# Optimization experiments

Measured on AMD Instinct MI355X. Metric: run time of the kernel, lower is better.

## Reference

```python
import jax, jax.numpy as jnp
import numpy as np

L, H, E, T, B, V = 8, 16, 1024, 1024, 2, 800
D = E // H  # head_size = 64
STD = 0.02


def setup_inputs() -> dict:
    key = jax.random.key(0)
    ks = iter(jax.random.split(key, 32))

    def nrm(shape):
        return jax.random.normal(next(ks), shape, jnp.float32) * STD

    latlong = jax.random.uniform(next(ks), (B, T, 2), jnp.float32)
    wl = jax.random.uniform(next(ks), (B, T, 1), jnp.float32, minval=3.0, maxval=11.0)
    inp = {
        "idx": jnp.concatenate([latlong, wl], axis=-1),  # [B,T,3]
        "tok_table": nrm((V, E)),
        "pos_W": nrm((2, E)),
        "pos_b": jnp.zeros((E,), jnp.float32),
        # stacked per-layer params (per-head q/k/v linears fused into [E,E])
        "Wq": nrm((L, E, E)),
        "Wk": nrm((L, E, E)),
        "Wv": nrm((L, E, E)),
        "Wo": nrm((L, E, E)),
        "bo": jnp.zeros((L, E), jnp.float32),
        "W1": nrm((L, E, 4 * E)),
        "b1": jnp.zeros((L, 4 * E), jnp.float32),
        "W2": nrm((L, 4 * E, E)),
        "b2": jnp.zeros((L, E), jnp.float32),
        "ln1_g": jnp.ones((L, E), jnp.float32),
        "ln1_b": jnp.zeros((L, E), jnp.float32),
        "ln2_g": jnp.ones((L, E), jnp.float32),
        "ln2_b": jnp.zeros((L, E), jnp.float32),
        "lnf_g": jnp.ones((E,), jnp.float32),
        "lnf_b": jnp.zeros((E,), jnp.float32),
        "lm_W": nrm((E, V)),
        "lm_b": jnp.zeros((V,), jnp.float32),
    }
    return inp


def _ln(x, g, b, eps=1e-5):
    m = x.mean(-1, keepdims=True)
    v = x.var(-1, keepdims=True)
    return (x - m) * jax.lax.rsqrt(v + eps) * g + b


def _block(x, p):
    Wq, Wk, Wv, Wo, bo, W1, b1, W2, b2, g1, be1, g2, be2 = p
    Bx, Tx, _ = x.shape
    h = _ln(x, g1, be1)
    q = (h @ Wq).reshape(Bx, Tx, H, D)
    k = (h @ Wk).reshape(Bx, Tx, H, D)
    v = (h @ Wv).reshape(Bx, Tx, H, D)
    scores = jnp.einsum('bqhd,bkhd->bhqk', q, k) * (D ** -0.5)
    mask = jnp.tril(jnp.ones((Tx, Tx), bool))  # causal
    scores = jnp.where(mask, scores, -jnp.inf)
    w = jax.nn.softmax(scores, axis=-1)  # dropout=0 (eval) -> identity
    attn = jnp.einsum('bhqk,bkhd->bqhd', w, v).reshape(Bx, Tx, E)
    x = x + attn @ Wo + bo
    h = _ln(x, g2, be2)
    x = x + jax.nn.relu(h @ W1 + b1) @ W2 + b2
    return x


def reference(idx, tok_table, pos_W, pos_b, Wq, Wk, Wv, Wo, bo, W1, b1, W2, b2,
              ln1_g, ln1_b, ln2_g, ln2_b, lnf_g, lnf_b, lm_W, lm_b):
    # water level channel -> token id in [0, V-1]
    idx_wl = jnp.clip(jnp.round(idx[..., 2] * 100.0 - 300.0), 0, V - 1).astype(jnp.int32)
    tok_emb = tok_table[idx_wl]                      # [B,T,E]
    pos_emb = idx[..., :2] @ pos_W + pos_b           # [B,T,E]
    x = tok_emb + pos_emb

    params = (Wq, Wk, Wv, Wo, bo, W1, b1, W2, b2, ln1_g, ln1_b, ln2_g, ln2_b)

    def body(carry, p):
        return _block(carry, p), None

    x, _ = jax.lax.scan(body, x, params)
    x = _ln(x, lnf_g, lnf_b)
    logits = x @ lm_W + lm_b                         # [B,T,V]
    return logits
```

## Files before the change

kernel.cpp:

```cpp
#include <hip/hip_runtime.h>
#include <hip/hip_bf16.h>

#define L_ 8
#define H_ 16
#define E_ 1024
#define T_ 1024
#define B_ 2
#define V_ 800
#define D_ 64
#define FF_ 4096
#define N_ (B_ * T_)
#define QS_ 3072

typedef unsigned short u16;
typedef __bf16 bf16x8 __attribute__((ext_vector_type(8)));
typedef float f32x4 __attribute__((ext_vector_type(4)));

__device__ __forceinline__ u16 f2b(float f) {
    unsigned int u = __float_as_uint(f);
    unsigned int r = (u + 0x7fffu + ((u >> 16) & 1u)) >> 16;
    return (u16)r;
}

__device__ __forceinline__ void gld16(const u16* g, u16* l) {
    __builtin_amdgcn_global_load_lds(
        (__attribute__((address_space(1))) void*)(uintptr_t)g,
        (__attribute__((address_space(3))) void*)(unsigned)(uintptr_t)l,
        16, 0, 0);
}

__global__ __launch_bounds__(256) void embed_k(
    const float* __restrict__ idx, const float* __restrict__ tok,
    const float* __restrict__ posW, const float* __restrict__ posb,
    float* __restrict__ x)
{
    int row = blockIdx.x;
    int e = threadIdx.x * 4;
    float lat = idx[row * 3 + 0];
    float lon = idx[row * 3 + 1];
    float wl  = idx[row * 3 + 2];
    float tf = rintf(wl * 100.0f - 300.0f);
    tf = fminf(fmaxf(tf, 0.0f), (float)(V_ - 1));
    int tkn = (int)tf;

    float4 tv = *(const float4*)(tok + (size_t)tkn * E_ + e);
    float4 p0 = *(const float4*)(posW + e);
    float4 p1 = *(const float4*)(posW + E_ + e);
    float4 pb = *(const float4*)(posb + e);
    float4 ov;
    ov.x = tv.x + lat * p0.x + lon * p1.x + pb.x;
    ov.y = tv.y + lat * p0.y + lon * p1.y + pb.y;
    ov.z = tv.z + lat * p0.z + lon * p1.z + pb.z;
    ov.w = tv.w + lat * p0.w + lon * p1.w + pb.w;
    *(float4*)(x + (size_t)row * E_ + e) = ov;
}

__global__ __launch_bounds__(256) void ln_k(
    const float* __restrict__ x, const float* __restrict__ g,
    const float* __restrict__ bta, u16* __restrict__ out)
{
    __shared__ float rs[4], rq[4];
    int row = blockIdx.x;
    int tid = threadIdx.x;
    const float* xr = x + (size_t)row * E_;
    float4 xv = *(const float4*)(xr + tid * 4);
    float s = xv.x + xv.y + xv.z + xv.w;
    float q = xv.x * xv.x + xv.y * xv.y + xv.z * xv.z + xv.w * xv.w;
    #pragma unroll
    for (int off = 32; off; off >>= 1) {
        s += __shfl_xor(s, off, 64);
        q += __shfl_xor(q, off, 64);
    }
    int wv = tid >> 6, ln = tid & 63;
    if (ln == 0) { rs[wv] = s; rq[wv] = q; }
    __syncthreads();
    s = rs[0] + rs[1] + rs[2] + rs[3];
    q = rq[0] + rq[1] + rq[2] + rq[3];
    float mean = s * (1.0f / E_);
    float var  = q * (1.0f / E_) - mean * mean;
    float inv  = 1.0f / sqrtf(var + 1e-5f);
    int c = tid * 4;
    float4 gv = *(const float4*)(g + c);
    float4 bv = *(const float4*)(bta + c);
    ushort4 ov;
    ov.x = f2b((xv.x - mean) * inv * gv.x + bv.x);
    ov.y = f2b((xv.y - mean) * inv * gv.y + bv.y);
    ov.z = f2b((xv.z - mean) * inv * gv.z + bv.z);
    ov.w = f2b((xv.w - mean) * inv * gv.w + bv.w);
    *(ushort4*)(out + (size_t)row * E_ + c) = ov;
}

__global__ __launch_bounds__(256) void comb_ln_k(
    const float* __restrict__ Cp, const float* __restrict__ bias,
    float* __restrict__ x, const float* __restrict__ g,
    const float* __restrict__ bta, u16* __restrict__ hout)
{
    __shared__ float rs[4], rq[4];
    int row = blockIdx.x;
    int tid = threadIdx.x;
    int c = tid * 4;
    size_t off = (size_t)row * E_ + c;
    const size_t total = (size_t)N_ * E_;
    float4 p0 = *(const float4*)(Cp + off);
    float4 p1 = *(const float4*)(Cp + total + off);
    float4 p2 = *(const float4*)(Cp + 2 * total + off);
    float4 p3 = *(const float4*)(Cp + 3 * total + off);
    float4 xv = *(const float4*)(x + off);
    float4 bv = *(const float4*)(bias + c);
    xv.x += p0.x + p1.x + p2.x + p3.x + bv.x;
    xv.y += p0.y + p1.y + p2.y + p3.y + bv.y;
    xv.z += p0.z + p1.z + p2.z + p3.z + bv.z;
    xv.w += p0.w + p1.w + p2.w + p3.w + bv.w;
    *(float4*)(x + off) = xv;

    float s = xv.x + xv.y + xv.z + xv.w;
    float q = xv.x * xv.x + xv.y * xv.y + xv.z * xv.z + xv.w * xv.w;
    #pragma unroll
    for (int o = 32; o; o >>= 1) {
        s += __shfl_xor(s, o, 64);
        q += __shfl_xor(q, o, 64);
    }
    int wv = tid >> 6, ln = tid & 63;
    if (ln == 0) { rs[wv] = s; rq[wv] = q; }
    __syncthreads();
    s = rs[0] + rs[1] + rs[2] + rs[3];
    q = rq[0] + rq[1] + rq[2] + rq[3];
    float mean = s * (1.0f / E_);
    float var  = q * (1.0f / E_) - mean * mean;
    float inv  = 1.0f / sqrtf(var + 1e-5f);
    float4 gv = *(const float4*)(g + c);
    float4 bb = *(const float4*)(bta + c);
    ushort4 ov;
    ov.x = f2b((xv.x - mean) * inv * gv.x + bb.x);
    ov.y = f2b((xv.y - mean) * inv * gv.y + bb.y);
    ov.z = f2b((xv.z - mean) * inv * gv.z + bb.z);
    ov.w = f2b((xv.w - mean) * inv * gv.w + bb.w);
    *(ushort4*)(hout + off) = ov;
}

__device__ __forceinline__ void wtrans_body(
    const float* __restrict__ W, u16* __restrict__ Wt, int K, int M,
    int m0, int k0)
{
    __shared__ float tile[64][65];
    int tid = threadIdx.x;
    int rr = tid >> 4, c4 = (tid & 15) * 4;
    if (m0 + 64 <= M) {
        #pragma unroll
        for (int p = 0; p < 4; p++) {
            int kk = rr + p * 16;
            float4 v4 = *(const float4*)(W + (size_t)(k0 + kk) * M + m0 + c4);
            tile[kk][c4 + 0] = v4.x; tile[kk][c4 + 1] = v4.y;
            tile[kk][c4 + 2] = v4.z; tile[kk][c4 + 3] = v4.w;
        }
    } else {
        #pragma unroll
        for (int p = 0; p < 4; p++) {
            int kk = rr + p * 16;
            const float* wr = W + (size_t)(k0 + kk) * M;
            #pragma unroll
            for (int c = 0; c < 4; c++) {
                int m = m0 + c4 + c;
                tile[kk][c4 + c] = (m < M) ? wr[m] : 0.0f;
            }
        }
    }
    __syncthreads();
    #pragma unroll
    for (int p = 0; p < 4; p++) {
        int ml = rr + p * 16;
        ushort4 o;
        o.x = f2b(tile[c4 + 0][ml]);
        o.y = f2b(tile[c4 + 1][ml]);
        o.z = f2b(tile[c4 + 2][ml]);
        o.w = f2b(tile[c4 + 3][ml]);
        *(ushort4*)(Wt + (size_t)(m0 + ml) * K + k0 + c4) = o;
    }
}

__global__ __launch_bounds__(256) void wtrans_k(
    const float* __restrict__ W, u16* __restrict__ Wt, int K, int M)
{
    wtrans_body(W, Wt, K, M, blockIdx.x * 64, blockIdx.y * 64);
}

__global__ __launch_bounds__(256) void wtrans_all_k(
    const float* __restrict__ Wq, const float* __restrict__ Wk,
    const float* __restrict__ Wv, const float* __restrict__ Wo,
    const float* __restrict__ W1, const float* __restrict__ W2,
    u16* __restrict__ wqkv_t, u16* __restrict__ wo_t,
    u16* __restrict__ w1_t, u16* __restrict__ w2_t)
{
    int bx = blockIdx.x, by = blockIdx.y, z = blockIdx.z;
    const size_t M1 = 1024 * 1024;
    if (z < 4) {
        if (bx >= 16) return;
        const float* W = (z == 0) ? Wq : (z == 1) ? Wk : (z == 2) ? Wv : Wo;
        u16* dst = (z < 3) ? (wqkv_t + (size_t)z * M1) : wo_t;
        wtrans_body(W, dst, E_, E_, bx * 64, by * 64);
    } else if (z == 4) {
        wtrans_body(W1, w1_t, E_, FF_, bx * 64, by * 64);
    } else {
        int id = by * 64 + bx;
        int mb = id >> 6, kb = id & 63;
        wtrans_body(W2, w2_t, FF_, E_, mb * 64, kb * 64);
    }
}

__global__ __launch_bounds__(256) void gemm_bf16(
    const u16* __restrict__ A, const u16* __restrict__ Bt,
    const float* __restrict__ bias, const float* __restrict__ res,
    float* __restrict__ Cf, u16* __restrict__ Cb, float* __restrict__ Cp,
    u16* __restrict__ VtOut, int K, int M, int relu)
{
    __shared__ __align__(16) u16 As[3][128 * 32];
    __shared__ __align__(16) u16 Bs[3][128 * 32];
    int tid = threadIdx.x;
    int bm = blockIdx.y * 128, bn = blockIdx.x * 128;
    int zz = blockIdx.z;
    int kslice = K / (int)gridDim.z;
    int lane = tid & 63, wv = tid >> 6;
    int l15 = lane & 15, q4 = lane >> 4;
    int wm = (wv & 1) * 64, wn = (wv >> 1) * 64;

    const u16* ga = A + (size_t)(bm + (tid >> 2)) * K + zz * kslice + (tid & 3) * 8;
    const u16* gb = Bt + (size_t)(bn + (tid >> 2)) * K + zz * kslice + (tid & 3) * 8;
    size_t gstep = (size_t)64 * K;
    int lofs = wv * (16 * 32);

    f32x4 acc[4][4];
    #pragma unroll
    for (int i = 0; i < 4; i++)
        #pragma unroll
        for (int j = 0; j < 4; j++)
            acc[i][j] = (f32x4){0.0f, 0.0f, 0.0f, 0.0f};

    auto STAGE = [&](int buf, int t) {
        const u16* a0 = ga + t * 32;
        const u16* b0 = gb + t * 32;
        u16* la = &As[buf][0] + lofs;
        u16* lb = &Bs[buf][0] + lofs;
        gld16(a0, la);
        gld16(a0 + gstep, la + 64 * 32);
        gld16(b0, lb);
        gld16(b0 + gstep, lb + 64 * 32);
    };

    int nt = kslice / 32;
    STAGE(0, 0);
    if (nt > 1) STAGE(1, 1);

    for (int t = 0; t < nt; ++t) {
        if (t + 1 < nt)
            asm volatile("s_waitcnt vmcnt(4) lgkmcnt(0)\n\ts_barrier" ::: "memory");
        else
            asm volatile("s_waitcnt vmcnt(0) lgkmcnt(0)\n\ts_barrier" ::: "memory");
        if (t + 2 < nt) STAGE((t + 2) % 3, t + 2);

        int cur = t % 3;
        const bf16x8* Ap = (const bf16x8*)(&As[cur][0]) + (wm + l15) * 4 + q4;
        const bf16x8* Bp = (const bf16x8*)(&Bs[cur][0]) + (wn + l15) * 4 + q4;
        bf16x8 af[4], bg[4];
        #pragma unroll
        for (int i = 0; i < 4; i++) { af[i] = Ap[i * 64]; bg[i] = Bp[i * 64]; }
        #pragma unroll
        for (int i = 0; i < 4; i++)
            #pragma unroll
            for (int j = 0; j < 4; j++)
                acc[i][j] = __builtin_amdgcn_mfma_f32_16x16x32_bf16(
                    af[i], bg[j], acc[i][j], 0, 0, 0);
    }

    size_t poff = (size_t)zz * N_ * M;
    #pragma unroll
    for (int i = 0; i < 4; i++) {
        int r0 = bm + wm + i * 16 + q4 * 4;
        #pragma unroll
        for (int j = 0; j < 4; j++) {
            int col = bn + wn + j * 16 + l15;
            if (col < M) {
                if (Cp) {
                    #pragma unroll
                    for (int r = 0; r < 4; r++)
                        Cp[poff + (size_t)(r0 + r) * M + col] = acc[i][j][r];
                } else {
                    float bv = bias ? bias[col] : 0.0f;
                    u16 vb[4];
                    #pragma unroll
                    for (int r = 0; r < 4; r++) {
                        size_t off = (size_t)(r0 + r) * M + col;
                        float v = acc[i][j][r] + bv;
                        if (res) v += res[off];
                        if (relu) v = fmaxf(v, 0.0f);
                        u16 hv = f2b(v);
                        vb[r] = hv;
                        if (Cb) Cb[off] = hv; else Cf[off] = v;
                    }
                    if (VtOut && col >= 2 * E_) {
                        int vcol = col - 2 * E_;
                        int hh = vcol >> 6, dd = vcol & 63;
                        int bb = r0 >> 10, t0 = r0 & 1023;
                        *(ushort4*)(VtOut +
                            ((size_t)(bb * H_ + hh) * D_ + dd) * T_ + t0) =
                            *(ushort4*)vb;
                    }
                }
            }
        }
    }
}

__global__ __launch_bounds__(256) void combine_k(
    const float* __restrict__ Cp, const float* __restrict__ bias,
    float* __restrict__ Cf, int M, int total)
{
    int e = (blockIdx.x * 256 + threadIdx.x) * 4;
    if (e >= total) return;
    float4 a = *(const float4*)(Cp + e);
    float4 b = *(const float4*)(Cp + (size_t)total + e);
    a.x += b.x; a.y += b.y; a.z += b.z; a.w += b.w;
    int col = e % M;
    if (bias) {
        float4 bv = *(const float4*)(bias + col);
        a.x += bv.x; a.y += bv.y; a.z += bv.z; a.w += bv.w;
    }
    *(float4*)(Cf + e) = a;
}

__global__ __launch_bounds__(256) void attn_mfma_k(
    const u16* __restrict__ QKV, const u16* __restrict__ Vt,
    u16* __restrict__ O)
{
    __shared__ __align__(16) u16 Ps[4][16 * 72];
    int tid = threadIdx.x;
    int wv = tid >> 6, lane = tid & 63;
    int c = lane & 15, q4 = lane >> 4;
    int qb = (int)(gridDim.x - 1) - (int)blockIdx.x;
    int h = blockIdx.y, b = blockIdx.z;
    int q0 = qb * 64 + wv * 16;
    const float scale = 0.125f;

    const u16* qrow = QKV + (size_t)(b * T_ + q0 + c) * QS_ + h * D_;
    bf16x8 qf0 = *(const bf16x8*)(qrow + q4 * 8);
    bf16x8 qf1 = *(const bf16x8*)(qrow + 32 + q4 * 8);

    const u16* kbase  = QKV + (size_t)b * T_ * QS_ + E_ + h * D_;
    const u16* vtbase = Vt + (size_t)(b * H_ + h) * D_ * T_;

    float l_acc[4] = {0.0f, 0.0f, 0.0f, 0.0f};
    f32x4 acc_o[4];
    #pragma unroll
    for (int nt = 0; nt < 4; nt++) acc_o[nt] = (f32x4){0.f, 0.f, 0.f, 0.f};

    u16* ps = &Ps[wv][0];

    for (int kt = 0; kt <= qb; kt++) {
        int k0 = kt * 64;
        bool diag = (kt == qb);

        bf16x8 kf[4][2];
        #pragma unroll
        for (int j = 0; j < 4; j++) {
            const u16* kr = kbase + (size_t)(k0 + 16 * j + c) * QS_ + q4 * 8;
            kf[j][0] = *(const bf16x8*)(kr);
            kf[j][1] = *(const bf16x8*)(kr + 32);
        }

        #pragma unroll
        for (int j = 0; j < 4; j++) {
            f32x4 sa = (f32x4){0.f, 0.f, 0.f, 0.f};
            sa = __builtin_amdgcn_mfma_f32_16x16x32_bf16(qf0, kf[j][0], sa, 0, 0, 0);
            sa = __builtin_amdgcn_mfma_f32_16x16x32_bf16(qf1, kf[j][1], sa, 0, 0, 0);
            #pragma unroll
            for (int r = 0; r < 4; r++) {
                bool masked = diag && (k0 + 16 * j + c > q0 + 4 * q4 + r);
                float pj = masked ? 0.0f : __expf(sa[r] * scale);
                l_acc[r] += pj;
                ps[(4 * q4 + r) * 72 + 16 * j + c] = f2b(pj);
            }
        }
        bf16x8 pf0 = *(const bf16x8*)(ps + c * 72 + q4 * 8);
        bf16x8 pf1 = *(const bf16x8*)(ps + c * 72 + 32 + q4 * 8);

        bf16x8 vf[4][2];
        #pragma unroll
        for (int nt = 0; nt < 4; nt++) {
            const u16* vr = vtbase + (size_t)(16 * nt + c) * T_ + k0 + q4 * 8;
            vf[nt][0] = *(const bf16x8*)(vr);
            vf[nt][1] = *(const bf16x8*)(vr + 32);
        }

        #pragma unroll
        for (int nt = 0; nt < 4; nt++) {
            acc_o[nt] = __builtin_amdgcn_mfma_f32_16x16x32_bf16(pf0, vf[nt][0], acc_o[nt], 0, 0, 0);
            acc_o[nt] = __builtin_amdgcn_mfma_f32_16x16x32_bf16(pf1, vf[nt][1], acc_o[nt], 0, 0, 0);
        }
    }

    #pragma unroll
    for (int r = 0; r < 4; r++) {
        float ts = l_acc[r];
        ts += __shfl_xor(ts, 1, 64);
        ts += __shfl_xor(ts, 2, 64);
        ts += __shfl_xor(ts, 4, 64);
        ts += __shfl_xor(ts, 8, 64);
        l_acc[r] = ts;
    }

    #pragma unroll
    for (int r = 0; r < 4; r++) {
        float inv = 1.0f / l_acc[r];
        size_t orow = (size_t)(b * T_ + q0 + 4 * q4 + r) * E_ + h * D_;
        #pragma unroll
        for (int nt = 0; nt < 4; nt++)
            O[orow + 16 * nt + c] = f2b(acc_o[nt][r] * inv);
    }
}

extern "C" void kernel_launch(void* const* d_in, const int* in_sizes, int n_in,
                              void* d_out, int out_size, void* d_ws, size_t ws_size,
                              hipStream_t stream)
{
    const float* idx   = (const float*)d_in[0];
    const float* tok   = (const float*)d_in[1];
    const float* posW  = (const float*)d_in[2];
    const float* posb  = (const float*)d_in[3];
    const float* Wq    = (const float*)d_in[4];
    const float* Wk    = (const float*)d_in[5];
    const float* Wv    = (const float*)d_in[6];
    const float* Wo    = (const float*)d_in[7];
    const float* bo    = (const float*)d_in[8];
    const float* W1    = (const float*)d_in[9];
    const float* b1    = (const float*)d_in[10];
    const float* W2    = (const float*)d_in[11];
    const float* b2    = (const float*)d_in[12];
    const float* ln1g  = (const float*)d_in[13];
    const float* ln1b  = (const float*)d_in[14];
    const float* ln2g  = (const float*)d_in[15];
    const float* ln2b  = (const float*)d_in[16];
    const float* lnfg  = (const float*)d_in[17];
    const float* lnfb  = (const float*)d_in[18];
    const float* lmW   = (const float*)d_in[19];
    const float* lmb   = (const float*)d_in[20];
    float* out = (float*)d_out;

    const size_t M1 = 1024 * 1024;
    float* ws    = (float*)d_ws;
    float* x     = ws;
    float* cpart = x + 2 * M1;
    u16* qkv   = (u16*)(cpart + 8 * M1);
    u16* vt    = qkv + 6 * M1;
    u16* h_bf  = vt + 2 * M1;
    u16* ao_bf = h_bf + 2 * M1;
    u16* ff_bf = ao_bf + 2 * M1;
    u16* wq_t  = ff_bf + 8 * M1;
    u16* wo_t  = wq_t + 3 * M1;
    u16* w1_t  = wo_t + 1 * M1;
    u16* w2_t  = w1_t + 4 * M1;
    u16* wlm_t = w2_t + 4 * M1;

    dim3 blk(256);
    dim3 gQKV(3072 / 128, N_ / 128, 1);
    dim3 gWo(1024 / 128, N_ / 128, 4);
    dim3 gW1(4096 / 128, N_ / 128, 1);
    dim3 gW2(1024 / 128, N_ / 128, 4);
    dim3 gLM(7, N_ / 128, 2);
    dim3 gAT(T_ / 64, H_, B_);
    dim3 gWT(64, 16, 6);
    dim3 tLM(14, 16);
    int totLM = N_ * V_;
    dim3 cLM(totLM / 4 / 256);

    embed_k<<<N_, blk, 0, stream>>>(idx, tok, posW, posb, x);
    ln_k<<<N_, blk, 0, stream>>>(x, ln1g, ln1b, h_bf);

    for (int l = 0; l < L_; l++) {
        size_t oEE = (size_t)l * E_ * E_;
        size_t oE  = (size_t)l * E_;
        size_t oEF = (size_t)l * E_ * FF_;
        size_t oF  = (size_t)l * FF_;

        wtrans_all_k<<<gWT, blk, 0, stream>>>(
            Wq + oEE, Wk + oEE, Wv + oEE, Wo + oEE, W1 + oEF, W2 + oEF,
            wq_t, wo_t, w1_t, w2_t);
        gemm_bf16<<<gQKV, blk, 0, stream>>>(h_bf, wq_t, nullptr, nullptr,
                                            nullptr, qkv, nullptr, vt, E_, QS_, 0);
        attn_mfma_k<<<gAT, blk, 0, stream>>>(qkv, vt, ao_bf);
        gemm_bf16<<<gWo, blk, 0, stream>>>(ao_bf, wo_t, nullptr, nullptr,
                                           nullptr, nullptr, cpart, nullptr, E_, E_, 0);
        comb_ln_k<<<N_, blk, 0, stream>>>(cpart, bo + oE, x,
                                          ln2g + oE, ln2b + oE, h_bf);
        gemm_bf16<<<gW1, blk, 0, stream>>>(h_bf, w1_t, b1 + oF, nullptr,
                                           nullptr, ff_bf, nullptr, nullptr, E_, FF_, 1);
        gemm_bf16<<<gW2, blk, 0, stream>>>(ff_bf, w2_t, nullptr, nullptr,
                                           nullptr, nullptr, cpart, nullptr, FF_, E_, 0);
        if (l < L_ - 1) {
            comb_ln_k<<<N_, blk, 0, stream>>>(cpart, b2 + oE, x,
                                              ln1g + oE + E_, ln1b + oE + E_, h_bf);
        } else {
            comb_ln_k<<<N_, blk, 0, stream>>>(cpart, b2 + oE, x,
                                              lnfg, lnfb, h_bf);
        }
    }

    wtrans_k<<<tLM, blk, 0, stream>>>(lmW, wlm_t, E_, V_);
    gemm_bf16<<<gLM, blk, 0, stream>>>(h_bf, wlm_t, nullptr, nullptr,
                                       nullptr, nullptr, cpart, nullptr, E_, V_, 0);
    combine_k<<<cLM, blk, 0, stream>>>(cpart, lmb, out, V_, totLM);
}
```

Before: 1.858 ms.

## Batch weight transposes, atomic split-K residual adds, XCD block remap, MFMA priority

```diff
diff --git a/kernel.cpp b/kernel.cpp
--- a/kernel.cpp
+++ b/kernel.cpp
@@ -29,13 +29,16 @@
         16, 0, 0);
 }
 
-__global__ __launch_bounds__(256) void embed_k(
+__global__ __launch_bounds__(256) void embed_ln_k(
     const float* __restrict__ idx, const float* __restrict__ tok,
     const float* __restrict__ posW, const float* __restrict__ posb,
-    float* __restrict__ x)
-{
+    const float* __restrict__ g, const float* __restrict__ bta,
+    float* __restrict__ x, u16* __restrict__ out)
+{
+    __shared__ float rs[4], rq[4];
     int row = blockIdx.x;
-    int e = threadIdx.x * 4;
+    int tid = threadIdx.x;
+    int e = tid * 4;
     float lat = idx[row * 3 + 0];
     float lon = idx[row * 3 + 1];
     float wl  = idx[row * 3 + 2];
@@ -47,12 +50,36 @@
     float4 p0 = *(const float4*)(posW + e);
     float4 p1 = *(const float4*)(posW + E_ + e);
     float4 pb = *(const float4*)(posb + e);
-    float4 ov;
-    ov.x = tv.x + lat * p0.x + lon * p1.x + pb.x;
-    ov.y = tv.y + lat * p0.y + lon * p1.y + pb.y;
-    ov.z = tv.z + lat * p0.z + lon * p1.z + pb.z;
-    ov.w = tv.w + lat * p0.w + lon * p1.w + pb.w;
-    *(float4*)(x + (size_t)row * E_ + e) = ov;
+    float4 xv;
+    xv.x = tv.x + lat * p0.x + lon * p1.x + pb.x;
+    xv.y = tv.y + lat * p0.y + lon * p1.y + pb.y;
+    xv.z = tv.z + lat * p0.z + lon * p1.z + pb.z;
+    xv.w = tv.w + lat * p0.w + lon * p1.w + pb.w;
+    *(float4*)(x + (size_t)row * E_ + e) = xv;
+
+    float s = xv.x + xv.y + xv.z + xv.w;
+    float q = xv.x * xv.x + xv.y * xv.y + xv.z * xv.z + xv.w * xv.w;
+    #pragma unroll
+    for (int off = 32; off; off >>= 1) {
+        s += __shfl_xor(s, off, 64);
+        q += __shfl_xor(q, off, 64);
+    }
+    int wv = tid >> 6, ln = tid & 63;
+    if (ln == 0) { rs[wv] = s; rq[wv] = q; }
+    __syncthreads();
+    s = rs[0] + rs[1] + rs[2] + rs[3];
+    q = rq[0] + rq[1] + rq[2] + rq[3];
+    float mean = s * (1.0f / E_);
+    float var  = q * (1.0f / E_) - mean * mean;
+    float inv  = 1.0f / sqrtf(var + 1e-5f);
+    float4 gv = *(const float4*)(g + e);
+    float4 bv = *(const float4*)(bta + e);
+    ushort4 ov;
+    ov.x = f2b((xv.x - mean) * inv * gv.x + bv.x);
+    ov.y = f2b((xv.y - mean) * inv * gv.y + bv.y);
+    ov.z = f2b((xv.z - mean) * inv * gv.z + bv.z);
+    ov.w = f2b((xv.w - mean) * inv * gv.w + bv.w);
+    *(ushort4*)(out + (size_t)row * E_ + e) = ov;
 }
 
 __global__ __launch_bounds__(256) void ln_k(
@@ -90,54 +117,6 @@
     *(ushort4*)(out + (size_t)row * E_ + c) = ov;
 }
 
-__global__ __launch_bounds__(256) void comb_ln_k(
-    const float* __restrict__ Cp, const float* __restrict__ bias,
-    float* __restrict__ x, const float* __restrict__ g,
-    const float* __restrict__ bta, u16* __restrict__ hout)
-{
-    __shared__ float rs[4], rq[4];
-    int row = blockIdx.x;
-    int tid = threadIdx.x;
-    int c = tid * 4;
-    size_t off = (size_t)row * E_ + c;
-    const size_t total = (size_t)N_ * E_;
-    float4 p0 = *(const float4*)(Cp + off);
-    float4 p1 = *(const float4*)(Cp + total + off);
-    float4 p2 = *(const float4*)(Cp + 2 * total + off);
-    float4 p3 = *(const float4*)(Cp + 3 * total + off);
-    float4 xv = *(const float4*)(x + off);
-    float4 bv = *(const float4*)(bias + c);
-    xv.x += p0.x + p1.x + p2.x + p3.x + bv.x;
-    xv.y += p0.y + p1.y + p2.y + p3.y + bv.y;
-    xv.z += p0.z + p1.z + p2.z + p3.z + bv.z;
-    xv.w += p0.w + p1.w + p2.w + p3.w + bv.w;
-    *(float4*)(x + off) = xv;
-
-    float s = xv.x + xv.y + xv.z + xv.w;
-    float q = xv.x * xv.x + xv.y * xv.y + xv.z * xv.z + xv.w * xv.w;
-    #pragma unroll
-    for (int o = 32; o; o >>= 1) {
-        s += __shfl_xor(s, o, 64);
-        q += __shfl_xor(q, o, 64);
-    }
-    int wv = tid >> 6, ln = tid & 63;
-    if (ln == 0) { rs[wv] = s; rq[wv] = q; }
-    __syncthreads();
-    s = rs[0] + rs[1] + rs[2] + rs[3];
-    q = rq[0] + rq[1] + rq[2] + rq[3];
-    float mean = s * (1.0f / E_);
-    float var  = q * (1.0f / E_) - mean * mean;
-    float inv  = 1.0f / sqrtf(var + 1e-5f);
-    float4 gv = *(const float4*)(g + c);
-    float4 bb = *(const float4*)(bta + c);
-    ushort4 ov;
-    ov.x = f2b((xv.x - mean) * inv * gv.x + bb.x);
-    ov.y = f2b((xv.y - mean) * inv * gv.y + bb.y);
-    ov.z = f2b((xv.z - mean) * inv * gv.z + bb.z);
-    ov.w = f2b((xv.w - mean) * inv * gv.w + bb.w);
-    *(ushort4*)(hout + off) = ov;
-}
-
 __device__ __forceinline__ void wtrans_body(
     const float* __restrict__ W, u16* __restrict__ Wt, int K, int M,
     int m0, int k0)
@@ -178,45 +157,56 @@
     }
 }
 
-__global__ __launch_bounds__(256) void wtrans_k(
-    const float* __restrict__ W, u16* __restrict__ Wt, int K, int M)
-{
-    wtrans_body(W, Wt, K, M, blockIdx.x * 64, blockIdx.y * 64);
-}
-
-__global__ __launch_bounds__(256) void wtrans_all_k(
+__global__ __launch_bounds__(256) void wtrans_mega_k(
     const float* __restrict__ Wq, const float* __restrict__ Wk,
     const float* __restrict__ Wv, const float* __restrict__ Wo,
     const float* __restrict__ W1, const float* __restrict__ W2,
-    u16* __restrict__ wqkv_t, u16* __restrict__ wo_t,
-    u16* __restrict__ w1_t, u16* __restrict__ w2_t)
-{
+    const float* __restrict__ lmW,
+    u16* __restrict__ wts, u16* __restrict__ wlm_t)
+{
+    const size_t M1 = 1024 * 1024;
     int bx = blockIdx.x, by = blockIdx.y, z = blockIdx.z;
-    const size_t M1 = 1024 * 1024;
-    if (z < 4) {
+    if (z == 48) {
+        if (bx >= 14) return;
+        wtrans_body(lmW, wlm_t, E_, V_, bx * 64, by * 64);
+        return;
+    }
+    int l = z / 6, t = z % 6;
+    u16* wb = wts + (size_t)l * 12 * M1;
+    size_t oEE = (size_t)l * E_ * E_;
+    size_t oEF = (size_t)l * E_ * FF_;
+    if (t < 4) {
         if (bx >= 16) return;
-        const float* W = (z == 0) ? Wq : (z == 1) ? Wk : (z == 2) ? Wv : Wo;
-        u16* dst = (z < 3) ? (wqkv_t + (size_t)z * M1) : wo_t;
+        const float* W = (t == 0) ? (Wq + oEE) : (t == 1) ? (Wk + oEE)
+                       : (t == 2) ? (Wv + oEE) : (Wo + oEE);
+        u16* dst = (t < 3) ? (wb + (size_t)t * M1) : (wb + 3 * M1);
         wtrans_body(W, dst, E_, E_, bx * 64, by * 64);
-    } else if (z == 4) {
-        wtrans_body(W1, w1_t, E_, FF_, bx * 64, by * 64);
+    } else if (t == 4) {
+        wtrans_body(W1 + oEF, wb + 4 * M1, E_, FF_, bx * 64, by * 64);
     } else {
         int id = by * 64 + bx;
         int mb = id >> 6, kb = id & 63;
-        wtrans_body(W2, w2_t, FF_, E_, mb * 64, kb * 64);
+        wtrans_body(W2 + oEF, wb + 8 * M1, FF_, E_, mb * 64, kb * 64);
     }
 }
 
 __global__ __launch_bounds__(256) void gemm_bf16(
     const u16* __restrict__ A, const u16* __restrict__ Bt,
-    const float* __restrict__ bias, const float* __restrict__ res,
+    const float* __restrict__ bias,
     float* __restrict__ Cf, u16* __restrict__ Cb, float* __restrict__ Cp,
-    u16* __restrict__ VtOut, int K, int M, int relu)
+    float* __restrict__ Cx, u16* __restrict__ VtOut, int K, int M, int relu)
 {
     __shared__ __align__(16) u16 As[3][128 * 32];
     __shared__ __align__(16) u16 Bs[3][128 * 32];
     int tid = threadIdx.x;
-    int bm = blockIdx.y * 128, bn = blockIdx.x * 128;
+
+    int nx = gridDim.x, ny = gridDim.y;
+    int nwg = nx * ny, cpx = nwg >> 3;
+    int orig = blockIdx.y * nx + blockIdx.x;
+    int wgid = (orig & 7) * cpx + (orig >> 3);
+    int bxs = wgid / ny, bys = wgid % ny;
+    int bm = bys * 128, bn = bxs * 128;
+
     int zz = blockIdx.z;
     int kslice = K / (int)gridDim.z;
     int lane = tid & 63, wv = tid >> 6;
@@ -263,12 +253,14 @@
         bf16x8 af[4], bg[4];
         #pragma unroll
         for (int i = 0; i < 4; i++) { af[i] = Ap[i * 64]; bg[i] = Bp[i * 64]; }
+        __builtin_amdgcn_s_setprio(1);
         #pragma unroll
         for (int i = 0; i < 4; i++)
             #pragma unroll
             for (int j = 0; j < 4; j++)
                 acc[i][j] = __builtin_amdgcn_mfma_f32_16x16x32_bf16(
                     af[i], bg[j], acc[i][j], 0, 0, 0);
+        __builtin_amdgcn_s_setprio(0);
     }
 
     size_t poff = (size_t)zz * N_ * M;
@@ -283,6 +275,12 @@
                     #pragma unroll
                     for (int r = 0; r < 4; r++)
                         Cp[poff + (size_t)(r0 + r) * M + col] = acc[i][j][r];
+                } else if (Cx) {
+                    float bv = (bias && zz == 0) ? bias[col] : 0.0f;
+                    #pragma unroll
+                    for (int r = 0; r < 4; r++)
+                        atomicAdd(Cx + (size_t)(r0 + r) * M + col,
+                                  acc[i][j][r] + bv);
                 } else {
                     float bv = bias ? bias[col] : 0.0f;
                     u16 vb[4];
@@ -290,7 +288,6 @@
                     for (int r = 0; r < 4; r++) {
                         size_t off = (size_t)(r0 + r) * M + col;
                         float v = acc[i][j][r] + bv;
-                        if (res) v += res[off];
                         if (relu) v = fmaxf(v, 0.0f);
                         u16 hv = f2b(v);
                         vb[r] = hv;
@@ -448,16 +445,13 @@
     float* ws    = (float*)d_ws;
     float* x     = ws;
     float* cpart = x + 2 * M1;
-    u16* qkv   = (u16*)(cpart + 8 * M1);
+    u16* qkv   = (u16*)(cpart + 4 * M1);
     u16* vt    = qkv + 6 * M1;
     u16* h_bf  = vt + 2 * M1;
     u16* ao_bf = h_bf + 2 * M1;
     u16* ff_bf = ao_bf + 2 * M1;
-    u16* wq_t  = ff_bf + 8 * M1;
-    u16* wo_t  = wq_t + 3 * M1;
-    u16* w1_t  = wo_t + 1 * M1;
-    u16* w2_t  = w1_t + 4 * M1;
-    u16* wlm_t = w2_t + 4 * M1;
+    u16* wts   = ff_bf + 8 * M1;
+    u16* wlm_t = wts + 96 * M1;
 
     dim3 blk(256);
     dim3 gQKV(3072 / 128, N_ / 128, 1);
@@ -466,45 +460,41 @@
     dim3 gW2(1024 / 128, N_ / 128, 4);
     dim3 gLM(7, N_ / 128, 2);
     dim3 gAT(T_ / 64, H_, B_);
-    dim3 gWT(64, 16, 6);
-    dim3 tLM(14, 16);
+    dim3 gWT(64, 16, 49);
     int totLM = N_ * V_;
     dim3 cLM(totLM / 4 / 256);
 
-    embed_k<<<N_, blk, 0, stream>>>(idx, tok, posW, posb, x);
-    ln_k<<<N_, blk, 0, stream>>>(x, ln1g, ln1b, h_bf);
+    embed_ln_k<<<N_, blk, 0, stream>>>(idx, tok, posW, posb, ln1g, ln1b,
+                                       x, h_bf);
+    wtrans_mega_k<<<gWT, blk, 0, stream>>>(Wq, Wk, Wv, Wo, W1, W2, lmW,
+                                           wts, wlm_t);
 
     for (int l = 0; l < L_; l++) {
-        size_t oEE = (size_t)l * E_ * E_;
-        size_t oE  = (size_t)l * E_;
-        size_t oEF = (size_t)l * E_ * FF_;
-        size_t oF  = (size_t)l * FF_;
-
-        wtrans_all_k<<<gWT, blk, 0, stream>>>(
-            Wq + oEE, Wk + oEE, Wv + oEE, Wo + oEE, W1 + oEF, W2 + oEF,
-            wq_t, wo_t, w1_t, w2_t);
-        gemm_bf16<<<gQKV, blk, 0, stream>>>(h_bf, wq_t, nullptr, nullptr,
-                                            nullptr, qkv, nullptr, vt, E_, QS_, 0);
+        size_t oE = (size_t)l * E_;
+        size_t oF = (size_t)l * FF_;
+        u16* wq_l = wts + (size_t)l * 12 * M1;
+        u16* wo_l = wq_l + 3 * M1;
+        u16* w1_l = wq_l + 4 * M1;
+        u16* w2_l = wq_l + 8 * M1;
+
+        gemm_bf16<<<gQKV, blk, 0, stream>>>(h_bf, wq_l, nullptr,
+            nullptr, qkv, nullptr, nullptr, vt, E_, QS_, 0);
         attn_mfma_k<<<gAT, blk, 0, stream>>>(qkv, vt, ao_bf);
-        gemm_bf16<<<gWo, blk, 0, stream>>>(ao_bf, wo_t, nullptr, nullptr,
-                                           nullptr, nullptr, cpart, nullptr, E_, E_, 0);
-        comb_ln_k<<<N_, blk, 0, stream>>>(cpart, bo + oE, x,
-                                          ln2g + oE, ln2b + oE, h_bf);
-        gemm_bf16<<<gW1, blk, 0, stream>>>(h_bf, w1_t, b1 + oF, nullptr,
-                                           nullptr, ff_bf, nullptr, nullptr, E_, FF_, 1);
-        gemm_bf16<<<gW2, blk, 0, stream>>>(ff_bf, w2_t, nullptr, nullptr,
-                                           nullptr, nullptr, cpart, nullptr, FF_, E_, 0);
+        gemm_bf16<<<gWo, blk, 0, stream>>>(ao_bf, wo_l, bo + oE,
+            nullptr, nullptr, nullptr, x, nullptr, E_, E_, 0);
+        ln_k<<<N_, blk, 0, stream>>>(x, ln2g + oE, ln2b + oE, h_bf);
+        gemm_bf16<<<gW1, blk, 0, stream>>>(h_bf, w1_l, b1 + oF,
+            nullptr, ff_bf, nullptr, nullptr, nullptr, E_, FF_, 1);
+        gemm_bf16<<<gW2, blk, 0, stream>>>(ff_bf, w2_l, b2 + oE,
+            nullptr, nullptr, nullptr, x, nullptr, FF_, E_, 0);
         if (l < L_ - 1) {
-            comb_ln_k<<<N_, blk, 0, stream>>>(cpart, b2 + oE, x,
-                                              ln1g + oE + E_, ln1b + oE + E_, h_bf);
+            ln_k<<<N_, blk, 0, stream>>>(x, ln1g + oE + E_, ln1b + oE + E_, h_bf);
         } else {
-            comb_ln_k<<<N_, blk, 0, stream>>>(cpart, b2 + oE, x,
-                                              lnfg, lnfb, h_bf);
-        }
-    }
-
-    wtrans_k<<<tLM, blk, 0, stream>>>(lmW, wlm_t, E_, V_);
-    gemm_bf16<<<gLM, blk, 0, stream>>>(h_bf, wlm_t, nullptr, nullptr,
-                                       nullptr, nullptr, cpart, nullptr, E_, V_, 0);
+            ln_k<<<N_, blk, 0, stream>>>(x, lnfg, lnfb, h_bf);
+        }
+    }
+
+    gemm_bf16<<<gLM, blk, 0, stream>>>(h_bf, wlm_t, nullptr,
+        nullptr, nullptr, cpart, nullptr, nullptr, E_, V_, 0);
     combine_k<<<cLM, blk, 0, stream>>>(cpart, lmb, out, V_, totLM);
 }
```

Result: slower. 2.115 ms (+13.8%).
